# Performance work log

Hardware: AMD Instinct MI355X
Metric: run time of the kernel (lower is better)

## Reference

```python
import jax, jax.numpy as jnp
import numpy as np

N_CLASSES = 1000
FEAT_DIM = 256
N = 65536


def setup_inputs() -> dict:
    key = jax.random.key(0)
    k1, k2, k3 = jax.random.split(key, 3)
    gt = jax.random.randint(k1, (N, N_CLASSES), 0, 2, dtype=jnp.int32)
    features = jax.random.normal(k2, (N, FEAT_DIM), dtype=jnp.float32)
    centers = jax.random.normal(k3, (N_CLASSES, FEAT_DIM), dtype=jnp.float32)
    return {"gt": gt, "features": features, "centers": centers}


def reference(gt, features, centers):
    # loss = (1/N) * sum_c sum_{i : gt[i,c] > 0} ||features[i] - centers[c]||^2
    # Vectorized via ||f||^2 + ||c||^2 - 2 f.c  (replaces the per-class python loop)
    mask = (gt > 0).astype(features.dtype)                      # [N, C]
    f_sq = jnp.sum(features * features, axis=1)                 # [N]
    c_sq = jnp.sum(centers * centers, axis=1)                   # [C]
    cross = features @ centers.T                                # [N, C]
    dist = f_sq[:, None] + c_sq[None, :] - 2.0 * cross          # [N, C]
    num_instances = features.shape[0]
    return jnp.sum(mask * dist) / num_instances
```

## Files before the change

### kernel.cpp

```cpp
#include <hip/hip_runtime.h>
#include <hip/hip_bf16.h>
#include <stdint.h>

#define N_ROWS 65536
#define N_CLS  1000
#define KPAD   1024
#define FEAT   256
#define MT     64
#define BK     64
#define NIT    (KPAD/BK)
#define LDA    72
#define LDB    72

typedef short bf16x8 __attribute__((ext_vector_type(8)));
typedef float f32x4  __attribute__((ext_vector_type(4)));

__device__ __forceinline__ ushort f32_to_bf16_rne(float f) {
    union { float f; uint32_t u; } x; x.f = f;
    uint32_t u = x.u + 0x7FFFu + ((x.u >> 16) & 1u);
    return (ushort)(u >> 16);
}

__global__ __launch_bounds__(256) void prep_kernel(const float* __restrict__ centers,
                                                   ushort* __restrict__ centersT,
                                                   float* __restrict__ csq,
                                                   float* __restrict__ out) {
    const int c = blockIdx.x;
    const int n = threadIdx.x;
    float v = 0.f;
    if (c < N_CLS) v = centers[(size_t)c * FEAT + n];
    centersT[(size_t)n * KPAD + c] = f32_to_bf16_rne(v);
    float sq = v * v;
    #pragma unroll
    for (int off = 32; off > 0; off >>= 1) sq += __shfl_down(sq, off);
    __shared__ float red[4];
    if ((threadIdx.x & 63) == 0) red[threadIdx.x >> 6] = sq;
    __syncthreads();
    if (threadIdx.x == 0) {
        csq[c] = red[0] + red[1] + red[2] + red[3];
        if (c == 0) out[0] = 0.f;
    }
}

__global__ __launch_bounds__(256) void main_kernel(const int* __restrict__ gt,
                                                   const float* __restrict__ features,
                                                   const ushort* __restrict__ centersT,
                                                   const float* __restrict__ csq,
                                                   float* __restrict__ out) {
    __shared__ ushort As[MT * LDA];
    __shared__ ushort Bs[FEAT * LDB];
    __shared__ float  rcS[256];
    __shared__ float  t2S[256];
    __shared__ float  rowcnt[MT];
    __shared__ float  t2row[MT];
    __shared__ float  blockred[4];

    const int tid  = threadIdx.x;
    const int m0   = blockIdx.x * MT;
    const int r    = tid >> 2;
    const int kc   = tid & 3;
    const int lane = tid & 63;
    const int w    = tid >> 6;
    const int ml   = lane & 15;
    const int quad = lane >> 4;

    f32x4 acc[4][4];
    #pragma unroll
    for (int i = 0; i < 4; i++)
        #pragma unroll
        for (int j = 0; j < 4; j++)
            #pragma unroll
            for (int k = 0; k < 4; k++) acc[i][j][k] = 0.f;

    float rc = 0.f, t2 = 0.f;
    const int* gtrow = gt + (size_t)(m0 + r) * N_CLS;

    for (int it = 0; it < NIT; ++it) {
        const int k0 = it * BK;
        __syncthreads();

        const int kb = k0 + kc * 16;
        int v[16];
        if (kb + 16 <= N_CLS) {
            const int4* p = (const int4*)(gtrow + kb);
            int4 a0 = p[0], a1 = p[1], a2 = p[2], a3 = p[3];
            v[0]=a0.x; v[1]=a0.y; v[2]=a0.z; v[3]=a0.w;
            v[4]=a1.x; v[5]=a1.y; v[6]=a1.z; v[7]=a1.w;
            v[8]=a2.x; v[9]=a2.y; v[10]=a2.z; v[11]=a2.w;
            v[12]=a3.x; v[13]=a3.y; v[14]=a3.z; v[15]=a3.w;
        } else {
            #pragma unroll
            for (int j = 0; j < 16; j++) {
                int k = kb + j;
                v[j] = (k < N_CLS) ? gtrow[k] : 0;
            }
        }
        float cs[16];
        {
            const float4* cp = (const float4*)(csq + kb);
            float4 q0 = cp[0], q1 = cp[1], q2 = cp[2], q3 = cp[3];
            cs[0]=q0.x; cs[1]=q0.y; cs[2]=q0.z; cs[3]=q0.w;
            cs[4]=q1.x; cs[5]=q1.y; cs[6]=q1.z; cs[7]=q1.w;
            cs[8]=q2.x; cs[9]=q2.y; cs[10]=q2.z; cs[11]=q2.w;
            cs[12]=q3.x; cs[13]=q3.y; cs[14]=q3.z; cs[15]=q3.w;
        }
        uint32_t u[8];
        #pragma unroll
        for (int j = 0; j < 8; j++) {
            uint32_t lo = (v[2*j]   > 0) ? 0x3F80u : 0u;
            uint32_t hi = (v[2*j+1] > 0) ? 0x3F80u : 0u;
            u[j] = lo | (hi << 16);
        }
        #pragma unroll
        for (int j = 0; j < 16; j++) {
            bool m = v[j] > 0;
            rc += m ? 1.f : 0.f;
            t2 += m ? cs[j] : 0.f;
        }
        {
            uint4* dst = (uint4*)&As[r * LDA + kc * 16];
            dst[0] = make_uint4(u[0], u[1], u[2], u[3]);
            dst[1] = make_uint4(u[4], u[5], u[6], u[7]);
        }

        #pragma unroll
        for (int j = 0; j < 8; j++) {
            int g = j * 256 + tid;
            int n = g >> 3;
            int kcb = g & 7;
            *(uint4*)&Bs[n * LDB + kcb * 8] =
                *(const uint4*)&centersT[(size_t)n * KPAD + k0 + kcb * 8];
        }

        __syncthreads();

        #pragma unroll
        for (int ks = 0; ks < 2; ++ks) {
            const int kk = ks * 32 + quad * 8;
            bf16x8 af[4], bfr[4];
            #pragma unroll
            for (int mt = 0; mt < 4; mt++)
                af[mt] = *(const bf16x8*)&As[(mt * 16 + ml) * LDA + kk];
            #pragma unroll
            for (int nt = 0; nt < 4; nt++)
                bfr[nt] = *(const bf16x8*)&Bs[(w * 64 + nt * 16 + ml) * LDB + kk];
            #pragma unroll
            for (int mt = 0; mt < 4; mt++)
                #pragma unroll
                for (int nt = 0; nt < 4; nt++)
                    acc[mt][nt] = __builtin_amdgcn_mfma_f32_16x16x32_bf16(
                        af[mt], bfr[nt], acc[mt][nt], 0, 0, 0);
        }
    }

    rcS[tid] = rc;
    t2S[tid] = t2;
    __syncthreads();
    if (tid < MT) {
        rowcnt[tid] = rcS[tid*4] + rcS[tid*4+1] + rcS[tid*4+2] + rcS[tid*4+3];
        t2row[tid]  = t2S[tid*4] + t2S[tid*4+1] + t2S[tid*4+2] + t2S[tid*4+3];
    }
    __syncthreads();

    float part = 0.f;
    #pragma unroll
    for (int mt = 0; mt < 4; mt++) {
        #pragma unroll
        for (int nt = 0; nt < 4; nt++) {
            const int n = w * 64 + nt * 16 + ml;
            #pragma unroll
            for (int reg = 0; reg < 4; reg++) {
                const int ri = mt * 16 + quad * 4 + reg;
                const float f = features[(size_t)(m0 + ri) * FEAT + n];
                const float T = acc[mt][nt][reg];
                part += f * (rowcnt[ri] * f - 2.f * T) + t2row[ri] * (1.f / 256.f);
            }
        }
    }
    #pragma unroll
    for (int off = 32; off > 0; off >>= 1) part += __shfl_down(part, off);
    if (lane == 0) blockred[w] = part;
    __syncthreads();
    if (tid == 0)
        atomicAdd(out, (blockred[0] + blockred[1] + blockred[2] + blockred[3]) *
                           (1.f / (float)N_ROWS));
}

extern "C" void kernel_launch(void* const* d_in, const int* in_sizes, int n_in,
                              void* d_out, int out_size, void* d_ws, size_t ws_size,
                              hipStream_t stream) {
    const int*   gt       = (const int*)d_in[0];
    const float* features = (const float*)d_in[1];
    const float* centers  = (const float*)d_in[2];
    float*       out      = (float*)d_out;

    ushort* centersT = (ushort*)d_ws;
    float*  csq      = (float*)((char*)d_ws + (size_t)FEAT * KPAD * 2);

    prep_kernel<<<KPAD, 256, 0, stream>>>(centers, centersT, csq, out);
    main_kernel<<<N_ROWS / MT, 256, 0, stream>>>(gt, features, centersT, csq, out);
}
```

Before: 412.0 us.

## Double-buffer gt tile, load centers fragments directly from global, simplify mask math

Drops the large shared-memory B tile and has each wave read its bf16 centers fragments straight from global/L2 into registers. The A (mask) tile is double-buffered: the next iteration's gt row is prefetched before the MFMAs and converted and stored afterwards, leaving one barrier per iteration. The mask conversion now uses integer multiply and add tricks, which assume gt values are exactly 0 or 1. Launch bounds request 3 blocks per CU. Freeing LDS should raise occupancy, at the cost of redundant global reads of centersT across blocks.

```diff
diff --git a/kernel.cpp b/kernel.cpp
--- a/kernel.cpp
+++ b/kernel.cpp
@@ -1,5 +1,4 @@
 #include <hip/hip_runtime.h>
-#include <hip/hip_bf16.h>
 #include <stdint.h>
 
 #define N_ROWS 65536
@@ -10,7 +9,6 @@
 #define BK     64
 #define NIT    (KPAD/BK)
 #define LDA    72
-#define LDB    72
 
 typedef short bf16x8 __attribute__((ext_vector_type(8)));
 typedef float f32x4  __attribute__((ext_vector_type(4)));
@@ -42,13 +40,12 @@
     }
 }
 
-__global__ __launch_bounds__(256) void main_kernel(const int* __restrict__ gt,
-                                                   const float* __restrict__ features,
-                                                   const ushort* __restrict__ centersT,
-                                                   const float* __restrict__ csq,
-                                                   float* __restrict__ out) {
-    __shared__ ushort As[MT * LDA];
-    __shared__ ushort Bs[FEAT * LDB];
+__global__ __launch_bounds__(256, 3) void main_kernel(const int* __restrict__ gt,
+                                                      const float* __restrict__ features,
+                                                      const ushort* __restrict__ centersT,
+                                                      const float* __restrict__ csq,
+                                                      float* __restrict__ out) {
+    __shared__ ushort As[2 * MT * LDA];
     __shared__ float  rcS[256];
     __shared__ float  t2S[256];
     __shared__ float  rowcnt[MT];
@@ -72,88 +69,94 @@
             #pragma unroll
             for (int k = 0; k < 4; k++) acc[i][j][k] = 0.f;
 
-    float rc = 0.f, t2 = 0.f;
+    int   rci = 0;
+    float t2  = 0.f;
     const int* gtrow = gt + (size_t)(m0 + r) * N_CLS;
 
-    for (int it = 0; it < NIT; ++it) {
-        const int k0 = it * BK;
-        __syncthreads();
-
-        const int kb = k0 + kc * 16;
-        int v[16];
+    auto load_gt = [&](int it, int (&vv)[16]) {
+        const int kb = it * BK + kc * 16;
         if (kb + 16 <= N_CLS) {
             const int4* p = (const int4*)(gtrow + kb);
             int4 a0 = p[0], a1 = p[1], a2 = p[2], a3 = p[3];
-            v[0]=a0.x; v[1]=a0.y; v[2]=a0.z; v[3]=a0.w;
-            v[4]=a1.x; v[5]=a1.y; v[6]=a1.z; v[7]=a1.w;
-            v[8]=a2.x; v[9]=a2.y; v[10]=a2.z; v[11]=a2.w;
-            v[12]=a3.x; v[13]=a3.y; v[14]=a3.z; v[15]=a3.w;
+            vv[0]=a0.x;  vv[1]=a0.y;  vv[2]=a0.z;  vv[3]=a0.w;
+            vv[4]=a1.x;  vv[5]=a1.y;  vv[6]=a1.z;  vv[7]=a1.w;
+            vv[8]=a2.x;  vv[9]=a2.y;  vv[10]=a2.z; vv[11]=a2.w;
+            vv[12]=a3.x; vv[13]=a3.y; vv[14]=a3.z; vv[15]=a3.w;
         } else {
             #pragma unroll
             for (int j = 0; j < 16; j++) {
                 int k = kb + j;
-                v[j] = (k < N_CLS) ? gtrow[k] : 0;
+                vv[j] = (k < N_CLS) ? gtrow[k] : 0;
             }
         }
-        float cs[16];
-        {
-            const float4* cp = (const float4*)(csq + kb);
-            float4 q0 = cp[0], q1 = cp[1], q2 = cp[2], q3 = cp[3];
-            cs[0]=q0.x; cs[1]=q0.y; cs[2]=q0.z; cs[3]=q0.w;
-            cs[4]=q1.x; cs[5]=q1.y; cs[6]=q1.z; cs[7]=q1.w;
-            cs[8]=q2.x; cs[9]=q2.y; cs[10]=q2.z; cs[11]=q2.w;
-            cs[12]=q3.x; cs[13]=q3.y; cs[14]=q3.z; cs[15]=q3.w;
-        }
+    };
+
+    auto convert_store = [&](int buf, int it, const int (&vv)[16]) {
+        const int kb = it * BK + kc * 16;
+        const float4* cp = (const float4*)(csq + kb);
+        float4 q0 = cp[0], q1 = cp[1], q2 = cp[2], q3 = cp[3];
+        float cs[16] = {q0.x,q0.y,q0.z,q0.w, q1.x,q1.y,q1.z,q1.w,
+                        q2.x,q2.y,q2.z,q2.w, q3.x,q3.y,q3.z,q3.w};
         uint32_t u[8];
         #pragma unroll
-        for (int j = 0; j < 8; j++) {
-            uint32_t lo = (v[2*j]   > 0) ? 0x3F80u : 0u;
-            uint32_t hi = (v[2*j+1] > 0) ? 0x3F80u : 0u;
-            u[j] = lo | (hi << 16);
-        }
+        for (int j = 0; j < 8; j++)
+            u[j] = (uint32_t)(vv[2*j] + (vv[2*j+1] << 16)) * 0x3F80u;
         #pragma unroll
         for (int j = 0; j < 16; j++) {
-            bool m = v[j] > 0;
-            rc += m ? 1.f : 0.f;
-            t2 += m ? cs[j] : 0.f;
-        }
-        {
-            uint4* dst = (uint4*)&As[r * LDA + kc * 16];
-            dst[0] = make_uint4(u[0], u[1], u[2], u[3]);
-            dst[1] = make_uint4(u[4], u[5], u[6], u[7]);
-        }
-
-        #pragma unroll
-        for (int j = 0; j < 8; j++) {
-            int g = j * 256 + tid;
-            int n = g >> 3;
-            int kcb = g & 7;
-            *(uint4*)&Bs[n * LDB + kcb * 8] =
-                *(const uint4*)&centersT[(size_t)n * KPAD + k0 + kcb * 8];
-        }
-
-        __syncthreads();
-
+            rci += vv[j];
+            t2  += (float)vv[j] * cs[j];
+        }
+        uint4* dst = (uint4*)&As[buf * (MT * LDA) + r * LDA + kc * 16];
+        dst[0] = make_uint4(u[0], u[1], u[2], u[3]);
+        dst[1] = make_uint4(u[4], u[5], u[6], u[7]);
+    };
+
+    {
+        int v0[16];
+        load_gt(0, v0);
+        convert_store(0, 0, v0);
+    }
+    __syncthreads();
+
+    int cur = 0;
+    const int nb = w * 64;
+    for (int it = 0; it < NIT; ++it) {
+        const bool hn = (it + 1 < NIT);
+
+        int vn[16];
+        if (hn) load_gt(it + 1, vn);
+
+        const int k0 = it * BK;
+        bf16x8 b0[4], b1[4];
+        #pragma unroll
+        for (int nt = 0; nt < 4; ++nt)
+            b0[nt] = *(const bf16x8*)&centersT[(size_t)(nb + nt*16 + ml) * KPAD + k0 + quad*8];
+        #pragma unroll
+        for (int nt = 0; nt < 4; ++nt)
+            b1[nt] = *(const bf16x8*)&centersT[(size_t)(nb + nt*16 + ml) * KPAD + k0 + 32 + quad*8];
+
+        const ushort* Ab = &As[cur * (MT * LDA)];
         #pragma unroll
         for (int ks = 0; ks < 2; ++ks) {
             const int kk = ks * 32 + quad * 8;
-            bf16x8 af[4], bfr[4];
+            bf16x8 af[4];
             #pragma unroll
             for (int mt = 0; mt < 4; mt++)
-                af[mt] = *(const bf16x8*)&As[(mt * 16 + ml) * LDA + kk];
-            #pragma unroll
-            for (int nt = 0; nt < 4; nt++)
-                bfr[nt] = *(const bf16x8*)&Bs[(w * 64 + nt * 16 + ml) * LDB + kk];
+                af[mt] = *(const bf16x8*)&Ab[(mt * 16 + ml) * LDA + kk];
             #pragma unroll
             for (int mt = 0; mt < 4; mt++)
                 #pragma unroll
                 for (int nt = 0; nt < 4; nt++)
                     acc[mt][nt] = __builtin_amdgcn_mfma_f32_16x16x32_bf16(
-                        af[mt], bfr[nt], acc[mt][nt], 0, 0, 0);
-        }
-    }
-
-    rcS[tid] = rc;
+                        af[mt], ks ? b1[nt] : b0[nt], acc[mt][nt], 0, 0, 0);
+        }
+
+        if (hn) convert_store(cur ^ 1, it + 1, vn);
+        __syncthreads();
+        cur ^= 1;
+    }
+
+    rcS[tid] = (float)rci;
     t2S[tid] = t2;
     __syncthreads();
     if (tid < MT) {
```

Result: slower. 434.0 us (+5.3%).

## Double the row tile, prefetch gt two iterations ahead, cache csq in LDS

Applied to the files above, without the earlier changes.

Each block now covers 128 rows with 512 threads. Eight waves are split into two row halves by four column quarters, so each staged B tile of centers serves twice as many rows. The gt mask loads are register double-buffered two iterations ahead so the global reads overlap the MFMA work. The csq vector now sits in shared memory, and the mask-to-bf16 conversion becomes a multiply, which assumes gt holds only 0 or 1. The trade-offs are more registers per thread (launch bounds of 2 blocks), more LDS, and the 0/1 assumption, which only holds for these inputs.

```diff
diff --git a/kernel.cpp b/kernel.cpp
--- a/kernel.cpp
+++ b/kernel.cpp
@@ -1,16 +1,16 @@
 #include <hip/hip_runtime.h>
-#include <hip/hip_bf16.h>
 #include <stdint.h>
 
 #define N_ROWS 65536
 #define N_CLS  1000
 #define KPAD   1024
 #define FEAT   256
-#define MT     64
+#define MT     128
 #define BK     64
 #define NIT    (KPAD/BK)
 #define LDA    72
 #define LDB    72
+#define NTHR   512
 
 typedef short bf16x8 __attribute__((ext_vector_type(8)));
 typedef float f32x4  __attribute__((ext_vector_type(4)));
@@ -42,18 +42,19 @@
     }
 }
 
-__global__ __launch_bounds__(256) void main_kernel(const int* __restrict__ gt,
-                                                   const float* __restrict__ features,
-                                                   const ushort* __restrict__ centersT,
-                                                   const float* __restrict__ csq,
-                                                   float* __restrict__ out) {
+__global__ __launch_bounds__(NTHR, 2) void main_kernel(const int* __restrict__ gt,
+                                                       const float* __restrict__ features,
+                                                       const ushort* __restrict__ centersT,
+                                                       const float* __restrict__ csq,
+                                                       float* __restrict__ out) {
     __shared__ ushort As[MT * LDA];
     __shared__ ushort Bs[FEAT * LDB];
-    __shared__ float  rcS[256];
-    __shared__ float  t2S[256];
+    __shared__ float  csqS[KPAD];
+    __shared__ float  rcS[NTHR];
+    __shared__ float  t2S[NTHR];
     __shared__ float  rowcnt[MT];
     __shared__ float  t2row[MT];
-    __shared__ float  blockred[4];
+    __shared__ float  blockred[8];
 
     const int tid  = threadIdx.x;
     const int m0   = blockIdx.x * MT;
@@ -61,6 +62,8 @@
     const int kc   = tid & 3;
     const int lane = tid & 63;
     const int w    = tid >> 6;
+    const int mh   = w >> 2;
+    const int wn   = w & 3;
     const int ml   = lane & 15;
     const int quad = lane >> 4;
 
@@ -75,75 +78,70 @@
     float rc = 0.f, t2 = 0.f;
     const int* gtrow = gt + (size_t)(m0 + r) * N_CLS;
 
-    for (int it = 0; it < NIT; ++it) {
-        const int k0 = it * BK;
-        __syncthreads();
-
-        const int kb = k0 + kc * 16;
-        int v[16];
+    auto load_gt = [&](int it, int4 (&d)[4]) {
+        const int kb = it * BK + kc * 16;
         if (kb + 16 <= N_CLS) {
             const int4* p = (const int4*)(gtrow + kb);
-            int4 a0 = p[0], a1 = p[1], a2 = p[2], a3 = p[3];
-            v[0]=a0.x; v[1]=a0.y; v[2]=a0.z; v[3]=a0.w;
-            v[4]=a1.x; v[5]=a1.y; v[6]=a1.z; v[7]=a1.w;
-            v[8]=a2.x; v[9]=a2.y; v[10]=a2.z; v[11]=a2.w;
-            v[12]=a3.x; v[13]=a3.y; v[14]=a3.z; v[15]=a3.w;
+            d[0] = p[0]; d[1] = p[1]; d[2] = p[2]; d[3] = p[3];
         } else {
+            int tmp[16];
             #pragma unroll
             for (int j = 0; j < 16; j++) {
                 int k = kb + j;
-                v[j] = (k < N_CLS) ? gtrow[k] : 0;
+                tmp[j] = (k < N_CLS) ? gtrow[k] : 0;
             }
-        }
-        float cs[16];
-        {
-            const float4* cp = (const float4*)(csq + kb);
-            float4 q0 = cp[0], q1 = cp[1], q2 = cp[2], q3 = cp[3];
-            cs[0]=q0.x; cs[1]=q0.y; cs[2]=q0.z; cs[3]=q0.w;
-            cs[4]=q1.x; cs[5]=q1.y; cs[6]=q1.z; cs[7]=q1.w;
-            cs[8]=q2.x; cs[9]=q2.y; cs[10]=q2.z; cs[11]=q2.w;
-            cs[12]=q3.x; cs[13]=q3.y; cs[14]=q3.z; cs[15]=q3.w;
-        }
+            d[0] = make_int4(tmp[0], tmp[1], tmp[2], tmp[3]);
+            d[1] = make_int4(tmp[4], tmp[5], tmp[6], tmp[7]);
+            d[2] = make_int4(tmp[8], tmp[9], tmp[10], tmp[11]);
+            d[3] = make_int4(tmp[12], tmp[13], tmp[14], tmp[15]);
+        }
+    };
+
+    auto convert_store = [&](int it, const int4 (&d)[4]) {
+        const int kb = it * BK + kc * 16;
+        const float4* cp = (const float4*)&csqS[kb];
+        float4 q0 = cp[0], q1 = cp[1], q2 = cp[2], q3 = cp[3];
+        float cs[16] = {q0.x,q0.y,q0.z,q0.w, q1.x,q1.y,q1.z,q1.w,
+                        q2.x,q2.y,q2.z,q2.w, q3.x,q3.y,q3.z,q3.w};
+        int v[16] = {d[0].x,d[0].y,d[0].z,d[0].w, d[1].x,d[1].y,d[1].z,d[1].w,
+                     d[2].x,d[2].y,d[2].z,d[2].w, d[3].x,d[3].y,d[3].z,d[3].w};
         uint32_t u[8];
         #pragma unroll
-        for (int j = 0; j < 8; j++) {
-            uint32_t lo = (v[2*j]   > 0) ? 0x3F80u : 0u;
-            uint32_t hi = (v[2*j+1] > 0) ? 0x3F80u : 0u;
-            u[j] = lo | (hi << 16);
-        }
+        for (int j = 0; j < 8; j++)
+            u[j] = (uint32_t)(v[2*j] + (v[2*j+1] << 16)) * 0x3F80u;
         #pragma unroll
         for (int j = 0; j < 16; j++) {
-            bool m = v[j] > 0;
-            rc += m ? 1.f : 0.f;
-            t2 += m ? cs[j] : 0.f;
-        }
-        {
-            uint4* dst = (uint4*)&As[r * LDA + kc * 16];
-            dst[0] = make_uint4(u[0], u[1], u[2], u[3]);
-            dst[1] = make_uint4(u[4], u[5], u[6], u[7]);
-        }
-
-        #pragma unroll
-        for (int j = 0; j < 8; j++) {
-            int g = j * 256 + tid;
+            rc += v[j] ? 1.f : 0.f;
+            t2 += v[j] ? cs[j] : 0.f;
+        }
+        uint4* dst = (uint4*)&As[r * LDA + kc * 16];
+        dst[0] = make_uint4(u[0], u[1], u[2], u[3]);
+        dst[1] = make_uint4(u[4], u[5], u[6], u[7]);
+    };
+
+    auto stage_B = [&](int it) {
+        const int k0 = it * BK;
+        #pragma unroll
+        for (int j = 0; j < 4; j++) {
+            int g = j * NTHR + tid;
             int n = g >> 3;
             int kcb = g & 7;
             *(uint4*)&Bs[n * LDB + kcb * 8] =
                 *(const uint4*)&centersT[(size_t)n * KPAD + k0 + kcb * 8];
         }
-
-        __syncthreads();
-
+    };
+
+    auto mfma_iter = [&]() {
         #pragma unroll
         for (int ks = 0; ks < 2; ++ks) {
             const int kk = ks * 32 + quad * 8;
             bf16x8 af[4], bfr[4];
             #pragma unroll
             for (int mt = 0; mt < 4; mt++)
-                af[mt] = *(const bf16x8*)&As[(mt * 16 + ml) * LDA + kk];
+                af[mt] = *(const bf16x8*)&As[(mh * 64 + mt * 16 + ml) * LDA + kk];
             #pragma unroll
             for (int nt = 0; nt < 4; nt++)
-                bfr[nt] = *(const bf16x8*)&Bs[(w * 64 + nt * 16 + ml) * LDB + kk];
+                bfr[nt] = *(const bf16x8*)&Bs[(wn * 64 + nt * 16 + ml) * LDB + kk];
             #pragma unroll
             for (int mt = 0; mt < 4; mt++)
                 #pragma unroll
@@ -151,6 +149,28 @@
                     acc[mt][nt] = __builtin_amdgcn_mfma_f32_16x16x32_bf16(
                         af[mt], bfr[nt], acc[mt][nt], 0, 0, 0);
         }
+    };
+
+    int4 P[4], Q[4];
+    *(float2*)&csqS[tid * 2] = *(const float2*)&csq[tid * 2];
+    load_gt(0, P);
+    load_gt(1, Q);
+    __syncthreads();
+
+    for (int it = 0; it < NIT; it += 2) {
+        convert_store(it, P);
+        stage_B(it);
+        if (it + 2 < NIT) load_gt(it + 2, P);
+        __syncthreads();
+        mfma_iter();
+        __syncthreads();
+
+        convert_store(it + 1, Q);
+        stage_B(it + 1);
+        if (it + 3 < NIT) load_gt(it + 3, Q);
+        __syncthreads();
+        mfma_iter();
+        __syncthreads();
     }
 
     rcS[tid] = rc;
@@ -167,10 +187,10 @@
     for (int mt = 0; mt < 4; mt++) {
         #pragma unroll
         for (int nt = 0; nt < 4; nt++) {
-            const int n = w * 64 + nt * 16 + ml;
+            const int n = wn * 64 + nt * 16 + ml;
             #pragma unroll
             for (int reg = 0; reg < 4; reg++) {
-                const int ri = mt * 16 + quad * 4 + reg;
+                const int ri = mh * 64 + mt * 16 + quad * 4 + reg;
                 const float f = features[(size_t)(m0 + ri) * FEAT + n];
                 const float T = acc[mt][nt][reg];
                 part += f * (rowcnt[ri] * f - 2.f * T) + t2row[ri] * (1.f / 256.f);
@@ -181,9 +201,11 @@
     for (int off = 32; off > 0; off >>= 1) part += __shfl_down(part, off);
     if (lane == 0) blockred[w] = part;
     __syncthreads();
-    if (tid == 0)
-        atomicAdd(out, (blockred[0] + blockred[1] + blockred[2] + blockred[3]) *
-                           (1.f / (float)N_ROWS));
+    if (tid == 0) {
+        float s = blockred[0] + blockred[1] + blockred[2] + blockred[3]
+                + blockred[4] + blockred[5] + blockred[6] + blockred[7];
+        atomicAdd(out, s * (1.f / (float)N_ROWS));
+    }
 }
 
 extern "C" void kernel_launch(void* const* d_in, const int* in_sizes, int n_in,
@@ -198,5 +220,5 @@
     float*  csq      = (float*)((char*)d_ws + (size_t)FEAT * KPAD * 2);
 
     prep_kernel<<<KPAD, 256, 0, stream>>>(centers, centersT, csq, out);
-    main_kernel<<<N_ROWS / MT, 256, 0, stream>>>(gt, features, centersT, csq, out);
-}
+    main_kernel<<<N_ROWS / MT, NTHR, 0, stream>>>(gt, features, centersT, csq, out);
+}
```

Result: no change. 412.8 us (+0.2%).
